# Kernel tuning notes

Measured on AMD Instinct MI355X. Metric: run time of the kernel, lower is better.

Reference implementation:

```python
import jax, jax.numpy as jnp
import numpy as np

KS = 3          # kernel_size
PAD = KS // 2   # =1, symmetric pad (pd=2, pdr=1 in the original)


def setup_inputs() -> dict:
    key = jax.random.key(0)
    k1, k2 = jax.random.split(key)
    B, H, W, T, C = 1, 48, 48, 48, 32
    q = jax.random.normal(k1, (B, H, W, T, C), dtype=jnp.float32)
    k = jax.random.normal(k2, (B, H, W, T, C), dtype=jnp.float32)
    return {"q": q, "k": k}


def reference(q, k):
    # q, k: [B, H, W, T, C]
    B, H, W, T, C = q.shape
    # zero-pad k spatially by 1 on each side (matches nnf.pad with pdr=1)
    kp = jnp.pad(k, ((0, 0), (PAD, PAD), (PAD, PAD), (PAD, PAD), (0, 0)))
    # gather the 27 shifted windows; token order (dh major, dt minor) matches
    # unfold(1).unfold(2).unfold(3) + permute in the original.
    wins = jnp.stack(
        [kp[:, a:a + H, b:b + W, c:c + T, :]
         for a in range(KS) for b in range(KS) for c in range(KS)],
        axis=4,
    )  # [B, H, W, T, 27, C]
    # QK^T over channel dim -> [B, H, W, T, 27]
    scores = jnp.einsum('bhwtc,bhwtjc->bhwtj', q, wins)
    attn = jax.nn.softmax(scores, axis=-1)
    # fixed displacement grid v: offsets (-1,0,1)^3 in (dh, dw, dt) order
    ax = jnp.arange(-(KS // 2), KS // 2 + 1, dtype=q.dtype)  # [-1, 0, 1]
    offs = jnp.stack(jnp.meshgrid(ax, ax, ax, indexing='ij'), axis=-1)
    offs = offs.reshape(KS ** 3, 3)  # [27, 3]
    # displacement-weighted sum -> [B, H, W, T, 3]
    x = jnp.einsum('bhwtj,jd->bhwtd', attn, offs)
    # -> [B, 3, H, W, T]
    return jnp.transpose(x, (0, 4, 1, 2, 3))
```

## Files before the change

### kernel.cpp

```cpp
#include <hip/hip_runtime.h>
#include <hip/hip_bf16.h>
#include <math.h>

#define DH 48
#define DW 48
#define DT 48
#define DC 32
#define NPOS (DH * DW * DT)

typedef float f32x2 __attribute__((ext_vector_type(2)));

template <int CTRL>
__device__ __forceinline__ float qperm_add(float v) {
    const int s = __builtin_amdgcn_update_dpp(
        0, __float_as_int(v), CTRL, 0xF, 0xF, true);
    return v + __int_as_float(s);
}

__device__ __forceinline__ float dot16(const float4 a0, const float4 a1,
                                       const float4 a2, const float4 a3,
                                       const float4 b0, const float4 b1,
                                       const float4 b2, const float4 b3) {
    f32x2 acc = {0.f, 0.f};
    acc = __builtin_elementwise_fma((f32x2){a0.x, a0.y}, (f32x2){b0.x, b0.y}, acc);
    acc = __builtin_elementwise_fma((f32x2){a0.z, a0.w}, (f32x2){b0.z, b0.w}, acc);
    acc = __builtin_elementwise_fma((f32x2){a1.x, a1.y}, (f32x2){b1.x, b1.y}, acc);
    acc = __builtin_elementwise_fma((f32x2){a1.z, a1.w}, (f32x2){b1.z, b1.w}, acc);
    acc = __builtin_elementwise_fma((f32x2){a2.x, a2.y}, (f32x2){b2.x, b2.y}, acc);
    acc = __builtin_elementwise_fma((f32x2){a2.z, a2.w}, (f32x2){b2.z, b2.w}, acc);
    acc = __builtin_elementwise_fma((f32x2){a3.x, a3.y}, (f32x2){b3.x, b3.y}, acc);
    acc = __builtin_elementwise_fma((f32x2){a3.z, a3.w}, (f32x2){b3.z, b3.w}, acc);
    return acc.x + acc.y;
}

__global__ __launch_bounds__(256, 4) void cotr_natt_kernel(
    const float* __restrict__ q,
    const float* __restrict__ k,
    float* __restrict__ out)
{
    const int tid = threadIdx.x;
    const int sub = tid & 1;
    const int col = tid >> 1;
    const int ct  = col & 1;
    const int cw  = (col >> 1) & 7;
    const int ch2 = col >> 4;

    const int bt = blockIdx.x % (DT / 4);
    const int bw = (blockIdx.x / (DT / 4)) % (DW / 8);
    const int bh = blockIdx.x / ((DT / 4) * (DW / 8));

    const int h = bh * 8 + ch2;
    const int w = bw * 8 + cw;
    const int tb = bt * 4 + ct * 2;

    const int idx0 = (h * DW + w) * DT + tb;

    const float4* qp0 =
        reinterpret_cast<const float4*>(q + (size_t)idx0 * DC) + sub * 4;
    const float4 qA0 = qp0[0], qA1 = qp0[1], qA2 = qp0[2], qA3 = qp0[3];
    const float4 qB0 = qp0[8], qB1 = qp0[9], qB2 = qp0[10], qB3 = qp0[11];

    int ttc[4];
    float tv[4];
#pragma unroll
    for (int l = 0; l < 4; ++l) {
        const int tt = tb - 1 + l;
        ttc[l] = min(max(tt, 0), DT - 1);
        tv[l] = ((unsigned)tt < DT) ? 1.0f : 0.0f;
    }

    float s0 = 0.f, oh0 = 0.f, ow0 = 0.f, ot0 = 0.f;
    float s1 = 0.f, oh1 = 0.f, ow1 = 0.f, ot1 = 0.f;

#pragma unroll
    for (int a = 0; a < 3; ++a) {
        const int hh = h + a - 1;
        const float fa = ((unsigned)hh < DH) ? 1.0f : 0.0f;
        const int hc = min(max(hh, 0), DH - 1);
#pragma unroll
        for (int b = 0; b < 3; ++b) {
            const int ww = w + b - 1;
            const float fab = fa * (((unsigned)ww < DW) ? 1.0f : 0.0f);
            const int wc = min(max(ww, 0), DW - 1);
            const int rb = (hc * DW + wc) * DT;
#pragma unroll
            for (int l = 0; l < 4; ++l) {
                const float4* kp = reinterpret_cast<const float4*>(
                    k + (size_t)(rb + ttc[l]) * DC) + sub * 4;
                const float4 k0 = kp[0], k1 = kp[1], k2 = kp[2], k3 = kp[3];
                const float sc = fab * tv[l];
                if (l <= 2) {
                    float d = dot16(qA0, qA1, qA2, qA3, k0, k1, k2, k3);
                    d = qperm_add<0xB1>(d);
                    const float e = __expf(d * sc);
                    s0 += e;
                    if (a == 0) oh0 -= e;
                    if (a == 2) oh0 += e;
                    if (b == 0) ow0 -= e;
                    if (b == 2) ow0 += e;
                    if (l == 0) ot0 -= e;
                    if (l == 2) ot0 += e;
                }
                if (l >= 1) {
                    float d = dot16(qB0, qB1, qB2, qB3, k0, k1, k2, k3);
                    d = qperm_add<0xB1>(d);
                    const float e = __expf(d * sc);
                    s1 += e;
                    if (a == 0) oh1 -= e;
                    if (a == 2) oh1 += e;
                    if (b == 0) ow1 -= e;
                    if (b == 2) ow1 += e;
                    if (l == 1) ot1 -= e;
                    if (l == 3) ot1 += e;
                }
            }
        }
    }

    const float i0 = 1.0f / s0;
    const float i1 = 1.0f / s1;

    if (sub == 0) {
        out[0 * NPOS + idx0]     = oh0 * i0;
        out[0 * NPOS + idx0 + 1] = oh1 * i1;
        out[1 * NPOS + idx0]     = ow0 * i0;
        out[1 * NPOS + idx0 + 1] = ow1 * i1;
    } else {
        out[2 * NPOS + idx0]     = ot0 * i0;
        out[2 * NPOS + idx0 + 1] = ot1 * i1;
    }
}

extern "C" void kernel_launch(void* const* d_in, const int* in_sizes, int n_in,
                              void* d_out, int out_size, void* d_ws, size_t ws_size,
                              hipStream_t stream) {
    const float* q = reinterpret_cast<const float*>(d_in[0]);
    const float* k = reinterpret_cast<const float*>(d_in[1]);
    float* out = reinterpret_cast<float*>(d_out);

    const int blocks = (DH / 8) * (DW / 8) * (DT / 4);
    cotr_natt_kernel<<<blocks, 256, 0, stream>>>(q, k, out);
}
```

Before: 87.51 us.

## Split channel dot across four lanes and reshape block tile to 4x4x8

Each output pair is now handled by four lanes instead of two, each covering 8 channels, with an extra DPP quad-permute reduction step. The block tile changes from 8x8x4 to 4x4x8 positions, giving more blocks and more threads in total. This lowers per-thread registers and load work and raises memory-level parallelism. In exchange, the exp and softmax arithmetic is duplicated across twice as many lanes and each reduction needs an extra cross-lane step.

```diff
diff --git a/kernel.cpp b/kernel.cpp
--- a/kernel.cpp
+++ b/kernel.cpp
@@ -17,19 +17,13 @@
     return v + __int_as_float(s);
 }
 
-__device__ __forceinline__ float dot16(const float4 a0, const float4 a1,
-                                       const float4 a2, const float4 a3,
-                                       const float4 b0, const float4 b1,
-                                       const float4 b2, const float4 b3) {
+__device__ __forceinline__ float dot8(const float4 a0, const float4 a1,
+                                      const float4 b0, const float4 b1) {
     f32x2 acc = {0.f, 0.f};
     acc = __builtin_elementwise_fma((f32x2){a0.x, a0.y}, (f32x2){b0.x, b0.y}, acc);
     acc = __builtin_elementwise_fma((f32x2){a0.z, a0.w}, (f32x2){b0.z, b0.w}, acc);
     acc = __builtin_elementwise_fma((f32x2){a1.x, a1.y}, (f32x2){b1.x, b1.y}, acc);
     acc = __builtin_elementwise_fma((f32x2){a1.z, a1.w}, (f32x2){b1.z, b1.w}, acc);
-    acc = __builtin_elementwise_fma((f32x2){a2.x, a2.y}, (f32x2){b2.x, b2.y}, acc);
-    acc = __builtin_elementwise_fma((f32x2){a2.z, a2.w}, (f32x2){b2.z, b2.w}, acc);
-    acc = __builtin_elementwise_fma((f32x2){a3.x, a3.y}, (f32x2){b3.x, b3.y}, acc);
-    acc = __builtin_elementwise_fma((f32x2){a3.z, a3.w}, (f32x2){b3.z, b3.w}, acc);
     return acc.x + acc.y;
 }
 
@@ -39,26 +33,25 @@
     float* __restrict__ out)
 {
     const int tid = threadIdx.x;
-    const int sub = tid & 1;
-    const int col = tid >> 1;
-    const int ct  = col & 1;
-    const int cw  = (col >> 1) & 7;
-    const int ch2 = col >> 4;
+    const int sub = tid & 3;
+    const int col = tid >> 2;
+    const int ct  = col & 3;
+    const int cw  = (col >> 2) & 3;
+    const int chh = col >> 4;
 
-    const int bt = blockIdx.x % (DT / 4);
-    const int bw = (blockIdx.x / (DT / 4)) % (DW / 8);
-    const int bh = blockIdx.x / ((DT / 4) * (DW / 8));
+    const int bt = blockIdx.x % (DT / 8);
+    const int bw = (blockIdx.x / (DT / 8)) % (DW / 4);
+    const int bh = blockIdx.x / ((DT / 8) * (DW / 4));
 
-    const int h = bh * 8 + ch2;
-    const int w = bw * 8 + cw;
-    const int tb = bt * 4 + ct * 2;
+    const int h = bh * 4 + chh;
+    const int w = bw * 4 + cw;
+    const int tb = bt * 8 + ct * 2;
 
     const int idx0 = (h * DW + w) * DT + tb;
 
-    const float4* qp0 =
-        reinterpret_cast<const float4*>(q + (size_t)idx0 * DC) + sub * 4;
-    const float4 qA0 = qp0[0], qA1 = qp0[1], qA2 = qp0[2], qA3 = qp0[3];
-    const float4 qB0 = qp0[8], qB1 = qp0[9], qB2 = qp0[10], qB3 = qp0[11];
+    const float4* qp = reinterpret_cast<const float4*>(q + (size_t)idx0 * DC);
+    const float4 qA0 = qp[sub * 2],     qA1 = qp[sub * 2 + 1];
+    const float4 qB0 = qp[8 + sub * 2], qB1 = qp[8 + sub * 2 + 1];
 
     int ttc[4];
     float tv[4];
@@ -86,12 +79,13 @@
 #pragma unroll
             for (int l = 0; l < 4; ++l) {
                 const float4* kp = reinterpret_cast<const float4*>(
-                    k + (size_t)(rb + ttc[l]) * DC) + sub * 4;
-                const float4 k0 = kp[0], k1 = kp[1], k2 = kp[2], k3 = kp[3];
+                    k + (size_t)(rb + ttc[l]) * DC);
+                const float4 k0 = kp[sub * 2], k1 = kp[sub * 2 + 1];
                 const float sc = fab * tv[l];
                 if (l <= 2) {
-                    float d = dot16(qA0, qA1, qA2, qA3, k0, k1, k2, k3);
+                    float d = dot8(qA0, qA1, k0, k1);
                     d = qperm_add<0xB1>(d);
+                    d = qperm_add<0x4E>(d);
                     const float e = __expf(d * sc);
                     s0 += e;
                     if (a == 0) oh0 -= e;
@@ -102,8 +96,9 @@
                     if (l == 2) ot0 += e;
                 }
                 if (l >= 1) {
-                    float d = dot16(qB0, qB1, qB2, qB3, k0, k1, k2, k3);
+                    float d = dot8(qB0, qB1, k0, k1);
                     d = qperm_add<0xB1>(d);
+                    d = qperm_add<0x4E>(d);
                     const float e = __expf(d * sc);
                     s1 += e;
                     if (a == 0) oh1 -= e;
@@ -123,9 +118,10 @@
     if (sub == 0) {
         out[0 * NPOS + idx0]     = oh0 * i0;
         out[0 * NPOS + idx0 + 1] = oh1 * i1;
+    } else if (sub == 1) {
         out[1 * NPOS + idx0]     = ow0 * i0;
         out[1 * NPOS + idx0 + 1] = ow1 * i1;
-    } else {
+    } else if (sub == 2) {
         out[2 * NPOS + idx0]     = ot0 * i0;
         out[2 * NPOS + idx0 + 1] = ot1 * i1;
     }
@@ -138,6 +134,6 @@
     const float* k = reinterpret_cast<const float*>(d_in[1]);
     float* out = reinterpret_cast<float*>(d_out);
 
-    const int blocks = (DH / 8) * (DW / 8) * (DT / 4);
+    const int blocks = (DH / 4) * (DW / 4) * (DT / 8);
     cotr_natt_kernel<<<blocks, 256, 0, stream>>>(q, k, out);
 }
```

After: 90.36 us. 3.3% more time.
